# Kernel optimization log

Measured on AMD Instinct MI355X. Metric: run time of the kernel, lower is better.

## Reference

```python
import jax, jax.numpy as jnp
import numpy as np

NUM_HEADS = 8
LN_EPS = 1e-5


def _comm_matrix(E):
    # chain graph: connection (i, i+1) with weight 0.5, symmetric
    cm = jnp.zeros((E, E), dtype=jnp.float32)
    idx = jnp.arange(E - 1)
    cm = cm.at[idx, idx + 1].set(0.5)
    return cm + cm.T


def setup_inputs() -> dict:
    key = jax.random.key(0)
    B, E, H = 2048, 16, 1024
    ks = jax.random.split(key, 8)
    s = 0.02
    return {
        "x": jax.random.normal(ks[0], (B, E, H), dtype=jnp.float32),
        "ln_g": jnp.ones((H,), jnp.float32),
        "ln_b": jnp.zeros((H,), jnp.float32),
        "wq": jax.random.normal(ks[1], (H, H), jnp.float32) * s,
        "bq": jnp.zeros((H,), jnp.float32),
        "wk": jax.random.normal(ks[2], (H, H), jnp.float32) * s,
        "bk": jnp.zeros((H,), jnp.float32),
        "wv": jax.random.normal(ks[3], (H, H), jnp.float32) * s,
        "bv": jnp.zeros((H,), jnp.float32),
        "wo": jax.random.normal(ks[4], (H, H), jnp.float32) * s,
        "bo": jnp.zeros((H,), jnp.float32),
        "wg": jax.random.normal(ks[5], (1, 2 * H), jnp.float32) * s,
        "bg": jnp.zeros((1,), jnp.float32),
    }


def reference(x, ln_g, ln_b, wq, bq, wk, bk, wv, bv, wo, bo, wg, bg):
    B, E, H = x.shape
    nh = NUM_HEADS
    hd = H // nh

    # --- graph communication: comm_matrix @ x over expert dim ---
    cm = _comm_matrix(E)                              # [E, E]
    comm = jnp.einsum('ef,bfh->beh', cm, x)           # [B, E, H]

    # --- cross-attention block (pre-LN, residual) ---
    residual = comm
    mu = comm.mean(-1, keepdims=True)
    var = comm.var(-1, keepdims=True)
    xn = (comm - mu) * jax.lax.rsqrt(var + LN_EPS) * ln_g + ln_b

    q = (xn @ wq.T + bq).reshape(B, E, nh, hd)
    k = (xn @ wk.T + bk).reshape(B, E, nh, hd)
    v = (xn @ wv.T + bv).reshape(B, E, nh, hd)

    scores = jnp.einsum('bqnd,bknd->bnqk', q, k) / (hd ** 0.5)  # [B, nh, E, E]
    attn = jax.nn.softmax(scores, axis=-1)
    attended = jnp.einsum('bnqk,bknd->bqnd', attn, v).reshape(B, E, H)
    comm_out = attended @ wo.T + bo + residual        # [B, E, H]

    # --- communication gate ---
    gate_in = jnp.concatenate([x, comm_out], axis=-1)  # [B, E, 2H]
    gate = jax.nn.sigmoid(gate_in @ wg.T + bg)         # [B, E, 1]
    return gate * comm_out + (1.0 - gate) * x
```

## Files before the change

kernel.cpp:

```cpp
#include <hip/hip_runtime.h>
#include <cstdint>
#include <cstddef>

#define HDIM 1024
#define EEXP 16
#define BATCH 2048
#define MROWS (BATCH * EEXP)
#define NHEADS 8
#define HEADD 128
#define KDIM 1024
#define LN_EPS 1e-5f

typedef __bf16 bf16x8_t __attribute__((ext_vector_type(8)));
typedef float f32x4_t __attribute__((ext_vector_type(4)));
typedef unsigned short u16x4_t __attribute__((ext_vector_type(4)));
typedef unsigned short u16x8_t __attribute__((ext_vector_type(8)));

__device__ __forceinline__ unsigned short f2bf(float f) {
    unsigned int u = __builtin_bit_cast(unsigned int, f);
    unsigned int r = (u + 0x7FFFu + ((u >> 16) & 1u)) >> 16;
    return (unsigned short)r;
}
__device__ __forceinline__ float bf2f(unsigned short h) {
    unsigned int u = ((unsigned int)h) << 16;
    return __builtin_bit_cast(float, u);
}

__global__ __launch_bounds__(256) void k_conv4(
    const float* __restrict__ s0, const float* __restrict__ s1,
    const float* __restrict__ s2, const float* __restrict__ s3,
    unsigned short* __restrict__ d0, unsigned short* __restrict__ d1,
    unsigned short* __restrict__ d2, unsigned short* __restrict__ d3) {
    const int which = blockIdx.x >> 10;
    const int i = ((blockIdx.x & 1023) * 256 + threadIdx.x) * 4;
    const float* s = (which == 0) ? s0 : (which == 1) ? s1 : (which == 2) ? s2 : s3;
    unsigned short* d = (which == 0) ? d0 : (which == 1) ? d1 : (which == 2) ? d2 : d3;
    float4 v = *(const float4*)(s + i);
    u16x4_t o;
    o.x = f2bf(v.x); o.y = f2bf(v.y); o.z = f2bf(v.z); o.w = f2bf(v.w);
    *(u16x4_t*)(d + i) = o;
}

__global__ __launch_bounds__(256) void k_prep(const float* __restrict__ x,
                                              const float* __restrict__ lng,
                                              const float* __restrict__ lnb,
                                              unsigned short* __restrict__ xn) {
    const int m = blockIdx.x;
    const int e = m & (EEXP - 1);
    const int t = threadIdx.x;
    const int h = t * 4;
    const float* xr = x + (size_t)m * HDIM;

    float c0 = 0.f, c1 = 0.f, c2 = 0.f, c3 = 0.f;
    if (e > 0) {
        float4 v = *(const float4*)(xr - HDIM + h);
        c0 = 0.5f * v.x; c1 = 0.5f * v.y; c2 = 0.5f * v.z; c3 = 0.5f * v.w;
    }
    if (e < EEXP - 1) {
        float4 v = *(const float4*)(xr + HDIM + h);
        c0 += 0.5f * v.x; c1 += 0.5f * v.y; c2 += 0.5f * v.z; c3 += 0.5f * v.w;
    }
    float s  = c0 + c1 + c2 + c3;
    float ss = c0 * c0 + c1 * c1 + c2 * c2 + c3 * c3;
#pragma unroll
    for (int off = 32; off; off >>= 1) {
        s  += __shfl_xor(s, off, 64);
        ss += __shfl_xor(ss, off, 64);
    }
    __shared__ float red[8];
    const int wv = t >> 6;
    if ((t & 63) == 0) { red[wv] = s; red[4 + wv] = ss; }
    __syncthreads();
    s  = red[0] + red[1] + red[2] + red[3];
    ss = red[4] + red[5] + red[6] + red[7];
    const float mean = s * (1.0f / HDIM);
    const float var  = ss * (1.0f / HDIM) - mean * mean;
    const float rinv = rsqrtf(var + LN_EPS);

    float4 g = *(const float4*)(lng + h);
    float4 b = *(const float4*)(lnb + h);
    u16x4_t o;
    o.x = f2bf((c0 - mean) * rinv * g.x + b.x);
    o.y = f2bf((c1 - mean) * rinv * g.y + b.y);
    o.z = f2bf((c2 - mean) * rinv * g.z + b.z);
    o.w = f2bf((c3 - mean) * rinv * g.w + b.w);
    *(u16x4_t*)(xn + (size_t)m * HDIM + h) = o;
}

template <int N, bool IS_QKV>
__global__ __launch_bounds__(256) void k_gemm(
    const unsigned short* __restrict__ A,
    const unsigned short* __restrict__ Bw,
    const float* __restrict__ b0,
    const float* __restrict__ b1,
    const float* __restrict__ b2,
    unsigned short* __restrict__ Cbf,
    float* __restrict__ Cf) {
    constexpr int K = KDIM;
    __shared__ unsigned short As[128 * 64];
    __shared__ unsigned short Bs[128 * 64];

    const int tid = threadIdx.x;
    const int xcd = blockIdx.x & 7;
    const int g   = blockIdx.x >> 3;
    int mt, nt;
    if constexpr (N == 3072) {
        const int st = g / 96, r = g % 96;
        mt = xcd * 32 + (st >> 1) * 8 + (r & 7);
        nt = (st & 1) * 12 + (r >> 3);
    } else {
        const int st = g >> 6, r = g & 63;
        mt = xcd * 32 + st * 8 + (r & 7);
        nt = r >> 3;
    }
    const int m0 = mt * 128, n0 = nt * 128;

    const int lane = tid & 63, wave = tid >> 6;
    const int wm   = (wave >> 1) * 64, wn = (wave & 1) * 64;
    const int quad = lane >> 4, r16 = lane & 15;
    const int srow = tid >> 3;
    const int sgk  = ((tid & 7) ^ (srow & 7)) * 8;

    f32x4_t acc[4][4];
#pragma unroll
    for (int i = 0; i < 4; i++)
#pragma unroll
        for (int j = 0; j < 4; j++) acc[i][j] = f32x4_t{0.f, 0.f, 0.f, 0.f};

    f32x4_t bias4[4];
#pragma unroll
    for (int j = 0; j < 4; j++) {
        const int col0 = n0 + wn + j * 16 + quad * 4;
        const float* bp;
        if constexpr (IS_QKV) {
            bp = (col0 < 1024) ? (b0 + col0)
               : (col0 < 2048) ? (b1 + col0 - 1024)
                               : (b2 + col0 - 2048);
        } else {
            bp = b0 + col0;
        }
        bias4[j] = *(const f32x4_t*)bp;
    }

    const unsigned short* Ag = A + (size_t)(m0 + srow) * K + sgk;
    const unsigned short* Bg = Bw + (size_t)(n0 + srow) * K + sgk;
    const int swz0 = ((0 * 4 + quad) ^ (r16 & 7)) * 8;
    const int swz1 = ((1 * 4 + quad) ^ (r16 & 7)) * 8;

    for (int k0 = 0; k0 < K; k0 += 64) {
        __syncthreads();
#pragma unroll
        for (int q = 0; q < 4; q++) {
            __builtin_amdgcn_global_load_lds(
                (const __attribute__((address_space(1))) void*)(Ag + (size_t)(q * 32) * K + k0),
                (__attribute__((address_space(3))) void*)(As + q * 2048 + tid * 8), 16, 0, 0);
        }
#pragma unroll
        for (int q = 0; q < 4; q++) {
            __builtin_amdgcn_global_load_lds(
                (const __attribute__((address_space(1))) void*)(Bg + (size_t)(q * 32) * K + k0),
                (__attribute__((address_space(3))) void*)(Bs + q * 2048 + tid * 8), 16, 0, 0);
        }
        __syncthreads();

#pragma unroll
        for (int h = 0; h < 2; h++) {
            const int swz = h ? swz1 : swz0;
            bf16x8_t a[4], b[4];
#pragma unroll
            for (int i = 0; i < 4; i++)
                a[i] = *(const bf16x8_t*)&As[(wm + i * 16 + r16) * 64 + swz];
#pragma unroll
            for (int j = 0; j < 4; j++)
                b[j] = *(const bf16x8_t*)&Bs[(wn + j * 16 + r16) * 64 + swz];
#pragma unroll
            for (int i = 0; i < 4; i++)
#pragma unroll
                for (int j = 0; j < 4; j++)
                    acc[i][j] = __builtin_amdgcn_mfma_f32_16x16x32_bf16(b[j], a[i], acc[i][j], 0, 0, 0);
        }
    }

#pragma unroll
    for (int i = 0; i < 4; i++) {
        const int grow = m0 + wm + i * 16 + r16;
#pragma unroll
        for (int j = 0; j < 4; j++) {
            const int col0 = n0 + wn + j * 16 + quad * 4;
            if constexpr (IS_QKV) {
                u16x4_t o;
                o.x = f2bf(acc[i][j][0] + bias4[j][0]);
                o.y = f2bf(acc[i][j][1] + bias4[j][1]);
                o.z = f2bf(acc[i][j][2] + bias4[j][2]);
                o.w = f2bf(acc[i][j][3] + bias4[j][3]);
                *(u16x4_t*)&Cbf[(size_t)grow * N + col0] = o;
            } else {
                f32x4_t o;
                o[0] = acc[i][j][0] + bias4[j][0];
                o[1] = acc[i][j][1] + bias4[j][1];
                o[2] = acc[i][j][2] + bias4[j][2];
                o[3] = acc[i][j][3] + bias4[j][3];
                *(f32x4_t*)&Cf[(size_t)grow * N + col0] = o;
            }
        }
    }
}

__global__ __launch_bounds__(256) void k_attn(const unsigned short* __restrict__ qkv,
                                              unsigned short* __restrict__ att) {
    const int bidx = blockIdx.x;
    const int b = bidx >> 3, n = bidx & 7;
    __shared__ float qs[16][132], ks[16][132], vs[16][132];
    __shared__ float ps[16][17];
    const int t = threadIdx.x;

    {
        const int row = t >> 4, c0 = (t & 15) * 8;
        const size_t base = (size_t)(b * EEXP + row) * (3 * HDIM) + n * HEADD + c0;
        u16x8_t qv = *(const u16x8_t*)&qkv[base];
        u16x8_t kv = *(const u16x8_t*)&qkv[base + HDIM];
        u16x8_t vv = *(const u16x8_t*)&qkv[base + 2 * HDIM];
        f32x4_t q0, q1, k0, k1, v0, v1;
#pragma unroll
        for (int u = 0; u < 4; u++) {
            q0[u] = bf2f(qv[u]); q1[u] = bf2f(qv[u + 4]);
            k0[u] = bf2f(kv[u]); k1[u] = bf2f(kv[u + 4]);
            v0[u] = bf2f(vv[u]); v1[u] = bf2f(vv[u + 4]);
        }
        *(f32x4_t*)&qs[row][c0] = q0; *(f32x4_t*)&qs[row][c0 + 4] = q1;
        *(f32x4_t*)&ks[row][c0] = k0; *(f32x4_t*)&ks[row][c0 + 4] = k1;
        *(f32x4_t*)&vs[row][c0] = v0; *(f32x4_t*)&vs[row][c0 + 4] = v1;
    }
    __syncthreads();

    const int qe = t >> 4, ke = t & 15;
    float s = 0.f;
#pragma unroll
    for (int d = 0; d < HEADD; d += 4) {
        f32x4_t qv = *(const f32x4_t*)&qs[qe][d];
        f32x4_t kv = *(const f32x4_t*)&ks[ke][d];
        s += qv[0] * kv[0] + qv[1] * kv[1] + qv[2] * kv[2] + qv[3] * kv[3];
    }
    s *= 0.08838834764831845f;
    float mx = s;
#pragma unroll
    for (int off = 8; off; off >>= 1) mx = fmaxf(mx, __shfl_xor(mx, off, 16));
    const float ex = __expf(s - mx);
    float sum = ex;
#pragma unroll
    for (int off = 8; off; off >>= 1) sum += __shfl_xor(sum, off, 16);
    ps[qe][ke] = ex / sum;
    __syncthreads();

    const int dd8 = (t & 15) * 8;
    float o[8] = {0.f, 0.f, 0.f, 0.f, 0.f, 0.f, 0.f, 0.f};
#pragma unroll
    for (int k2 = 0; k2 < EEXP; k2++) {
        const float p = ps[qe][k2];
        f32x4_t v0 = *(const f32x4_t*)&vs[k2][dd8];
        f32x4_t v1 = *(const f32x4_t*)&vs[k2][dd8 + 4];
        o[0] += p * v0[0]; o[1] += p * v0[1]; o[2] += p * v0[2]; o[3] += p * v0[3];
        o[4] += p * v1[0]; o[5] += p * v1[1]; o[6] += p * v1[2]; o[7] += p * v1[3];
    }
    u16x8_t ov;
#pragma unroll
    for (int u = 0; u < 8; u++) ov[u] = f2bf(o[u]);
    *(u16x8_t*)&att[(size_t)(b * EEXP + qe) * HDIM + n * HEADD + dd8] = ov;
}

__global__ __launch_bounds__(256) void k_gate(const float* __restrict__ x,
                                              const float* __restrict__ wg,
                                              const float* __restrict__ bg,
                                              float* __restrict__ out) {
    const int m = blockIdx.x;
    const int e = m & (EEXP - 1);
    const int t = threadIdx.x;
    const int h = t * 4;
    const float* xr = x + (size_t)m * HDIM;
    float* orow = out + (size_t)m * HDIM;

    float4 xv = *(const float4*)(xr + h);
    float4 rv = *(const float4*)(orow + h);
    float c0 = 0.f, c1 = 0.f, c2 = 0.f, c3 = 0.f;
    if (e > 0) {
        float4 v = *(const float4*)(xr - HDIM + h);
        c0 = 0.5f * v.x; c1 = 0.5f * v.y; c2 = 0.5f * v.z; c3 = 0.5f * v.w;
    }
    if (e < EEXP - 1) {
        float4 v = *(const float4*)(xr + HDIM + h);
        c0 += 0.5f * v.x; c1 += 0.5f * v.y; c2 += 0.5f * v.z; c3 += 0.5f * v.w;
    }
    const float co0 = rv.x + c0, co1 = rv.y + c1, co2 = rv.z + c2, co3 = rv.w + c3;

    float4 w1 = *(const float4*)(wg + h);
    float4 w2 = *(const float4*)(wg + HDIM + h);
    float d = xv.x * w1.x + xv.y * w1.y + xv.z * w1.z + xv.w * w1.w +
              co0 * w2.x + co1 * w2.y + co2 * w2.z + co3 * w2.w;
#pragma unroll
    for (int off = 32; off; off >>= 1) d += __shfl_xor(d, off, 64);
    __shared__ float red[4];
    const int wv = t >> 6;
    if ((t & 63) == 0) red[wv] = d;
    __syncthreads();
    const float tot = red[0] + red[1] + red[2] + red[3] + bg[0];
    const float gate = 1.0f / (1.0f + __expf(-tot));

    float4 ov;
    ov.x = gate * co0 + (1.0f - gate) * xv.x;
    ov.y = gate * co1 + (1.0f - gate) * xv.y;
    ov.z = gate * co2 + (1.0f - gate) * xv.z;
    ov.w = gate * co3 + (1.0f - gate) * xv.w;
    *(float4*)(orow + h) = ov;
}

extern "C" void kernel_launch(void* const* d_in, const int* in_sizes, int n_in,
                              void* d_out, int out_size, void* d_ws, size_t ws_size,
                              hipStream_t stream) {
    const float* x   = (const float*)d_in[0];
    const float* lng = (const float*)d_in[1];
    const float* lnb = (const float*)d_in[2];
    const float* wq  = (const float*)d_in[3];
    const float* bq  = (const float*)d_in[4];
    const float* wk  = (const float*)d_in[5];
    const float* bk  = (const float*)d_in[6];
    const float* wv  = (const float*)d_in[7];
    const float* bv  = (const float*)d_in[8];
    const float* wo  = (const float*)d_in[9];
    const float* bo  = (const float*)d_in[10];
    const float* wg  = (const float*)d_in[11];
    const float* bg  = (const float*)d_in[12];
    float* out = (float*)d_out;

    unsigned short* wqkv = (unsigned short*)d_ws;
    unsigned short* wob  = wqkv + (size_t)3072 * 1024;
    unsigned short* xn   = wob + (size_t)1024 * 1024;
    unsigned short* qkv  = xn + (size_t)MROWS * HDIM;
    unsigned short* att  = qkv + (size_t)MROWS * 3 * HDIM;

    const int WELTS = 1024 * 1024;
    k_conv4<<<4096, 256, 0, stream>>>(wq, wk, wv, wo,
                                      wqkv, wqkv + (size_t)WELTS,
                                      wqkv + (size_t)2 * WELTS, wob);

    k_prep<<<MROWS, 256, 0, stream>>>(x, lng, lnb, xn);

    k_gemm<3072, true><<<(MROWS / 128) * (3072 / 128), 256, 0, stream>>>(
        xn, wqkv, bq, bk, bv, qkv, nullptr);

    k_attn<<<BATCH * NHEADS, 256, 0, stream>>>(qkv, att);

    k_gemm<1024, false><<<(MROWS / 128) * (1024 / 128), 256, 0, stream>>>(
        att, wob, bo, nullptr, nullptr, nullptr, out);

    k_gate<<<MROWS, 256, 0, stream>>>(x, wg, bg, out);
}
```

Baseline: 788.2 us.

## Rewrite GEMM as 256x256 tiles with 8 waves and phased LDS pipelining

Replaces the 128x128, 4-wave GEMM with a 256x256-tile, 512-thread kernel. It uses a 128 KB shared buffer that holds double-buffered A and B slices, issued as global_load_lds in phases interleaved with MFMA work. Explicit vmcnt waits, raw barriers and setprio keep loads in flight while the matrix cores run, and the larger tile raises data reuse per byte loaded. The cost is much higher LDS and register pressure (one block per CU in practice) and hand-tuned wait counts that must match the staging order exactly.

```diff
diff --git a/kernel.cpp b/kernel.cpp
--- a/kernel.cpp
+++ b/kernel.cpp
@@ -88,7 +88,7 @@
 }
 
 template <int N, bool IS_QKV>
-__global__ __launch_bounds__(256) void k_gemm(
+__global__ __launch_bounds__(512, 2) void k_gemm2(
     const unsigned short* __restrict__ A,
     const unsigned short* __restrict__ Bw,
     const float* __restrict__ b0,
@@ -97,113 +97,175 @@
     unsigned short* __restrict__ Cbf,
     float* __restrict__ Cf) {
     constexpr int K = KDIM;
-    __shared__ unsigned short As[128 * 64];
-    __shared__ unsigned short Bs[128 * 64];
-
-    const int tid = threadIdx.x;
+    __shared__ unsigned short S[65536];
+
+    const int tid  = threadIdx.x;
+    const int lane = tid & 63;
+    const int wave = tid >> 6;
+    const int quad = lane >> 4, r16 = lane & 15;
+    const int wm2  = wave >> 2, wn4 = wave & 3;
+
     const int xcd = blockIdx.x & 7;
     const int g   = blockIdx.x >> 3;
     int mt, nt;
     if constexpr (N == 3072) {
-        const int st = g / 96, r = g % 96;
-        mt = xcd * 32 + (st >> 1) * 8 + (r & 7);
-        nt = (st & 1) * 12 + (r >> 3);
+        const int st = g / 48, r = g % 48;
+        mt = xcd * 16 + st * 4 + (r & 3);
+        nt = r >> 2;
     } else {
-        const int st = g >> 6, r = g & 63;
-        mt = xcd * 32 + st * 8 + (r & 7);
-        nt = r >> 3;
-    }
-    const int m0 = mt * 128, n0 = nt * 128;
-
-    const int lane = tid & 63, wave = tid >> 6;
-    const int wm   = (wave >> 1) * 64, wn = (wave & 1) * 64;
-    const int quad = lane >> 4, r16 = lane & 15;
-    const int srow = tid >> 3;
-    const int sgk  = ((tid & 7) ^ (srow & 7)) * 8;
-
-    f32x4_t acc[4][4];
-#pragma unroll
-    for (int i = 0; i < 4; i++)
-#pragma unroll
-        for (int j = 0; j < 4; j++) acc[i][j] = f32x4_t{0.f, 0.f, 0.f, 0.f};
+        const int st = g >> 4, r = g & 15;
+        mt = xcd * 16 + st * 4 + (r & 3);
+        nt = r >> 2;
+    }
+    const int m0 = mt * 256, n0 = nt * 256;
+
+    const int srow0 = tid >> 3;
+    const int gk = ((tid & 7) ^ (srow0 & 7)) * 8;
+    const unsigned short* Ag = A  + (size_t)(m0 + srow0) * K + gk;
+    const unsigned short* Bg = Bw + (size_t)(n0 + srow0) * K + gk;
+
+    const int swz0 = ((0 + quad) ^ (r16 & 7)) * 8;
+    const int swz1 = ((4 + quad) ^ (r16 & 7)) * 8;
+    const int aBase = wm2 * 8192 + r16 * 64;
+    const int bBase = (2 + (wn4 >> 1)) * 8192 + (wn4 & 1) * 4096 + r16 * 64;
+
+    f32x4_t acc[8][4];
+#pragma unroll
+    for (int f = 0; f < 8; ++f)
+#pragma unroll
+        for (int j = 0; j < 4; ++j) acc[f][j] = f32x4_t{0.f, 0.f, 0.f, 0.f};
+
+    bf16x8_t bfr[4][2];
+
+#define STG(reg, srcb, rowoff, kk0)                                                          \
+    do {                                                                                     \
+        __builtin_amdgcn_global_load_lds(                                                    \
+            (const __attribute__((address_space(1))) void*)((srcb) + (size_t)(rowoff) * K + (kk0)),       \
+            (__attribute__((address_space(3))) void*)(S + (reg) * 8192 + tid * 8), 16, 0, 0);             \
+        __builtin_amdgcn_global_load_lds(                                                    \
+            (const __attribute__((address_space(1))) void*)((srcb) + (size_t)((rowoff) + 64) * K + (kk0)),\
+            (__attribute__((address_space(3))) void*)(S + (reg) * 8192 + 4096 + tid * 8), 16, 0, 0);      \
+    } while (0)
+
+#define DSRD_B(buf)                                                                          \
+    do {                                                                                     \
+        _Pragma("unroll") for (int j = 0; j < 4; ++j) {                                      \
+            bfr[j][0] = *(const bf16x8_t*)&S[(buf) * 32768 + bBase + j * 1024 + swz0];       \
+            bfr[j][1] = *(const bf16x8_t*)&S[(buf) * 32768 + bBase + j * 1024 + swz1];       \
+        }                                                                                    \
+    } while (0)
+
+#define VM4 asm volatile("s_waitcnt vmcnt(4)" ::: "memory")
+#define VM0 asm volatile("s_waitcnt vmcnt(0)" ::: "memory")
+#define NOSTG ((void)0)
+#define NOWAIT ((void)0)
+
+#define PHASE(buf, ph, STAGE_STMT, WAIT_STMT)                                                \
+    do {                                                                                     \
+        bf16x8_t afr[2][2];                                                                  \
+        _Pragma("unroll") for (int s2 = 0; s2 < 2; ++s2) {                                   \
+            afr[s2][0] = *(const bf16x8_t*)&S[(buf) * 32768 + aBase + ((ph) * 2 + s2) * 1024 + swz0]; \
+            afr[s2][1] = *(const bf16x8_t*)&S[(buf) * 32768 + aBase + ((ph) * 2 + s2) * 1024 + swz1]; \
+        }                                                                                    \
+        STAGE_STMT;                                                                          \
+        WAIT_STMT;                                                                           \
+        __builtin_amdgcn_s_barrier();                                                        \
+        asm volatile("s_waitcnt lgkmcnt(0)" ::: "memory");                                   \
+        __builtin_amdgcn_s_setprio(1);                                                       \
+        _Pragma("unroll") for (int s2 = 0; s2 < 2; ++s2)                                     \
+            _Pragma("unroll") for (int j = 0; j < 4; ++j) {                                  \
+                acc[(ph) * 2 + s2][j] = __builtin_amdgcn_mfma_f32_16x16x32_bf16(             \
+                    bfr[j][0], afr[s2][0], acc[(ph) * 2 + s2][j], 0, 0, 0);                  \
+                acc[(ph) * 2 + s2][j] = __builtin_amdgcn_mfma_f32_16x16x32_bf16(             \
+                    bfr[j][1], afr[s2][1], acc[(ph) * 2 + s2][j], 0, 0, 0);                  \
+            }                                                                                \
+        __builtin_amdgcn_s_setprio(0);                                                       \
+        __builtin_amdgcn_s_barrier();                                                        \
+    } while (0)
+
+    STG(0, Ag, 0,   0);
+    STG(1, Ag, 128, 0);
+    STG(2, Bg, 0,   0);
+    STG(3, Bg, 128, 0);
+    STG(6, Bg, 0,   64);
+    STG(7, Bg, 128, 64);
+    VM4;
+    __builtin_amdgcn_s_barrier();
+
+#pragma unroll 1
+    for (int i = 0; i < 7; ++i) {
+        const int kA1 = (2 * i + 1) * 64;
+        const int kN2 = (2 * i + 2) * 64;
+        const int kN3 = (2 * i + 3) * 64;
+        DSRD_B(0);
+        PHASE(0, 0, STG(4, Ag, 0,   kA1), NOWAIT);
+        PHASE(0, 1, STG(5, Ag, 128, kA1), NOWAIT);
+        PHASE(0, 2, STG(2, Bg, 0,   kN2), NOWAIT);
+        PHASE(0, 3, STG(3, Bg, 128, kN2), VM4);
+        DSRD_B(1);
+        PHASE(1, 0, STG(0, Ag, 0,   kN2), NOWAIT);
+        PHASE(1, 1, STG(1, Ag, 128, kN2), NOWAIT);
+        PHASE(1, 2, STG(6, Bg, 0,   kN3), NOWAIT);
+        PHASE(1, 3, STG(7, Bg, 128, kN3), VM4);
+    }
+    {
+        DSRD_B(0);
+        PHASE(0, 0, STG(4, Ag, 0,   960), NOWAIT);
+        PHASE(0, 1, STG(5, Ag, 128, 960), NOWAIT);
+        PHASE(0, 2, NOSTG, NOWAIT);
+        PHASE(0, 3, NOSTG, VM0);
+        DSRD_B(1);
+        PHASE(1, 0, NOSTG, NOWAIT);
+        PHASE(1, 1, NOSTG, NOWAIT);
+        PHASE(1, 2, NOSTG, NOWAIT);
+        PHASE(1, 3, NOSTG, NOWAIT);
+    }
 
     f32x4_t bias4[4];
 #pragma unroll
-    for (int j = 0; j < 4; j++) {
-        const int col0 = n0 + wn + j * 16 + quad * 4;
+    for (int j = 0; j < 4; ++j) {
+        const int gcol = n0 + wn4 * 64 + j * 16 + quad * 4;
         const float* bp;
         if constexpr (IS_QKV) {
-            bp = (col0 < 1024) ? (b0 + col0)
-               : (col0 < 2048) ? (b1 + col0 - 1024)
-                               : (b2 + col0 - 2048);
+            bp = (gcol < 1024) ? (b0 + gcol)
+               : (gcol < 2048) ? (b1 + gcol - 1024)
+                               : (b2 + gcol - 2048);
         } else {
-            bp = b0 + col0;
+            bp = b0 + gcol;
         }
         bias4[j] = *(const f32x4_t*)bp;
     }
 
-    const unsigned short* Ag = A + (size_t)(m0 + srow) * K + sgk;
-    const unsigned short* Bg = Bw + (size_t)(n0 + srow) * K + sgk;
-    const int swz0 = ((0 * 4 + quad) ^ (r16 & 7)) * 8;
-    const int swz1 = ((1 * 4 + quad) ^ (r16 & 7)) * 8;
-
-    for (int k0 = 0; k0 < K; k0 += 64) {
-        __syncthreads();
-#pragma unroll
-        for (int q = 0; q < 4; q++) {
-            __builtin_amdgcn_global_load_lds(
-                (const __attribute__((address_space(1))) void*)(Ag + (size_t)(q * 32) * K + k0),
-                (__attribute__((address_space(3))) void*)(As + q * 2048 + tid * 8), 16, 0, 0);
-        }
-#pragma unroll
-        for (int q = 0; q < 4; q++) {
-            __builtin_amdgcn_global_load_lds(
-                (const __attribute__((address_space(1))) void*)(Bg + (size_t)(q * 32) * K + k0),
-                (__attribute__((address_space(3))) void*)(Bs + q * 2048 + tid * 8), 16, 0, 0);
-        }
-        __syncthreads();
-
-#pragma unroll
-        for (int h = 0; h < 2; h++) {
-            const int swz = h ? swz1 : swz0;
-            bf16x8_t a[4], b[4];
-#pragma unroll
-            for (int i = 0; i < 4; i++)
-                a[i] = *(const bf16x8_t*)&As[(wm + i * 16 + r16) * 64 + swz];
-#pragma unroll
-            for (int j = 0; j < 4; j++)
-                b[j] = *(const bf16x8_t*)&Bs[(wn + j * 16 + r16) * 64 + swz];
-#pragma unroll
-            for (int i = 0; i < 4; i++)
-#pragma unroll
-                for (int j = 0; j < 4; j++)
-                    acc[i][j] = __builtin_amdgcn_mfma_f32_16x16x32_bf16(b[j], a[i], acc[i][j], 0, 0, 0);
-        }
-    }
-
-#pragma unroll
-    for (int i = 0; i < 4; i++) {
-        const int grow = m0 + wm + i * 16 + r16;
-#pragma unroll
-        for (int j = 0; j < 4; j++) {
-            const int col0 = n0 + wn + j * 16 + quad * 4;
+#pragma unroll
+    for (int f = 0; f < 8; ++f) {
+        const int grow = m0 + wm2 * 128 + f * 16 + r16;
+#pragma unroll
+        for (int j = 0; j < 4; ++j) {
+            const int gcol = n0 + wn4 * 64 + j * 16 + quad * 4;
             if constexpr (IS_QKV) {
                 u16x4_t o;
-                o.x = f2bf(acc[i][j][0] + bias4[j][0]);
-                o.y = f2bf(acc[i][j][1] + bias4[j][1]);
-                o.z = f2bf(acc[i][j][2] + bias4[j][2]);
-                o.w = f2bf(acc[i][j][3] + bias4[j][3]);
-                *(u16x4_t*)&Cbf[(size_t)grow * N + col0] = o;
+                o.x = f2bf(acc[f][j][0] + bias4[j][0]);
+                o.y = f2bf(acc[f][j][1] + bias4[j][1]);
+                o.z = f2bf(acc[f][j][2] + bias4[j][2]);
+                o.w = f2bf(acc[f][j][3] + bias4[j][3]);
+                *(u16x4_t*)&Cbf[(size_t)grow * N + gcol] = o;
             } else {
                 f32x4_t o;
-                o[0] = acc[i][j][0] + bias4[j][0];
-                o[1] = acc[i][j][1] + bias4[j][1];
-                o[2] = acc[i][j][2] + bias4[j][2];
-                o[3] = acc[i][j][3] + bias4[j][3];
-                *(f32x4_t*)&Cf[(size_t)grow * N + col0] = o;
+                o[0] = acc[f][j][0] + bias4[j][0];
+                o[1] = acc[f][j][1] + bias4[j][1];
+                o[2] = acc[f][j][2] + bias4[j][2];
+                o[3] = acc[f][j][3] + bias4[j][3];
+                *(f32x4_t*)&Cf[(size_t)grow * N + gcol] = o;
             }
         }
     }
+#undef STG
+#undef DSRD_B
+#undef PHASE
+#undef VM4
+#undef VM0
+#undef NOSTG
+#undef NOWAIT
 }
 
 __global__ __launch_bounds__(256) void k_attn(const unsigned short* __restrict__ qkv,
@@ -344,12 +406,12 @@
 
     k_prep<<<MROWS, 256, 0, stream>>>(x, lng, lnb, xn);
 
-    k_gemm<3072, true><<<(MROWS / 128) * (3072 / 128), 256, 0, stream>>>(
+    k_gemm2<3072, true><<<(MROWS / 256) * (3072 / 256), 512, 0, stream>>>(
         xn, wqkv, bq, bk, bv, qkv, nullptr);
 
     k_attn<<<BATCH * NHEADS, 256, 0, stream>>>(qkv, att);
 
-    k_gemm<1024, false><<<(MROWS / 128) * (1024 / 128), 256, 0, stream>>>(
+    k_gemm2<1024, false><<<(MROWS / 256) * (1024 / 256), 512, 0, stream>>>(
         att, wob, bo, nullptr, nullptr, nullptr, out);
 
     k_gate<<<MROWS, 256, 0, stream>>>(x, wg, bg, out);
```

Result: faster. 707.4 us (-10.2%).
